# Kernel optimization log

Hardware: AMD Instinct MI355X
Metric: run time of the kernel (lower is better)

The kernel has to match this reference:

```python
import jax, jax.numpy as jnp
import numpy as np


def setup_inputs() -> dict:
    key = jax.random.key(0)
    ks = jax.random.split(key, 10)
    B, L, D_MODEL = 2, 2048, 1024
    D_INNER, N, W, R = 2048, 16, 4, 64
    s = 0.02
    return {
        "hidden_states": jax.random.normal(ks[0], (B, L, D_MODEL), jnp.float32),
        "in_proj_w": jax.random.normal(ks[1], (2 * D_INNER, D_MODEL), jnp.float32) * s,
        "conv_w": jax.random.normal(ks[2], (D_INNER, W), jnp.float32) * 0.2,
        "conv_b": jax.random.normal(ks[3], (D_INNER,), jnp.float32) * 0.02,
        "x_proj_w": jax.random.normal(ks[4], (R + 2 * N, D_INNER), jnp.float32) * s,
        "dt_proj_w": jax.random.normal(ks[5], (D_INNER, R), jnp.float32) * (R ** -0.5),
        "dt_proj_b": jnp.log(jnp.expm1(jnp.exp(jax.random.uniform(ks[6], (D_INNER,), jnp.float32, np.log(1e-3), np.log(1e-1)))) + 1e-20),
        "A_log": jnp.log(jnp.broadcast_to(jnp.arange(1, N + 1, dtype=jnp.float32), (D_INNER, N))),
        "D_param": jnp.ones((D_INNER,), jnp.float32),
        "out_proj_w": jax.random.normal(ks[7], (D_MODEL, D_INNER), jnp.float32) * s,
    }


def _mamba_fwd(hidden_states, in_proj_w, conv_w, conv_b, x_proj_w,
               dt_proj_w, dt_proj_b, A_log, D_param, out_proj_w):
    Bsz, L, _ = hidden_states.shape
    d_inner = conv_w.shape[0]
    n = A_log.shape[1]
    r = dt_proj_w.shape[1]

    # input projection -> x, z  (each [B, L, d_inner])
    xz = jnp.einsum('bld,ed->ble', hidden_states, in_proj_w)
    x, z = xz[..., :d_inner], xz[..., d_inner:]

    # depthwise causal conv over L with SiLU
    x_bdl = jnp.transpose(x, (0, 2, 1))  # [B, d, L]
    kern = conv_w[:, None, :]            # [d, 1, W]
    xc = jax.lax.conv_general_dilated(
        x_bdl, kern, window_strides=(1,), padding=[(conv_w.shape[1] - 1, 0)],
        dimension_numbers=('NCH', 'OIH', 'NCH'), feature_group_count=d_inner)
    xc = xc + conv_b[None, :, None]
    xc = xc * jax.nn.sigmoid(xc)         # silu, [B, d, L]
    u = jnp.transpose(xc, (0, 2, 1))     # [B, L, d]

    # SSM parameter projections
    x_dbl = jnp.einsum('bld,ed->ble', u, x_proj_w)   # [B, L, r+2n]
    dt_lo = x_dbl[..., :r]
    B_ssm = x_dbl[..., r:r + n]                       # [B, L, n]
    C_ssm = x_dbl[..., r + n:]                        # [B, L, n]
    delta = jax.nn.softplus(jnp.einsum('blr,dr->bld', dt_lo, dt_proj_w) + dt_proj_b)

    A = -jnp.exp(A_log)  # [d, n]

    # selective scan over time (sequential recurrence)
    def step(h, inp):
        d_t, u_t, b_t, c_t = inp  # [B,d], [B,d], [B,n], [B,n]
        dA = jnp.exp(d_t[..., None] * A)                       # [B,d,n]
        h = dA * h + (d_t * u_t)[..., None] * b_t[:, None, :]  # [B,d,n]
        y_t = jnp.einsum('bdn,bn->bd', h, c_t)
        return h, y_t

    h0 = jnp.zeros((Bsz, d_inner, n), dtype=u.dtype)
    xs = (jnp.transpose(delta, (1, 0, 2)), jnp.transpose(u, (1, 0, 2)),
          jnp.transpose(B_ssm, (1, 0, 2)), jnp.transpose(C_ssm, (1, 0, 2)))
    _, ys = jax.lax.scan(step, h0, xs)           # ys: [L, B, d]
    y = jnp.transpose(ys, (1, 0, 2)) + u * D_param
    y = y * (z * jax.nn.sigmoid(z))              # gate: y * silu(z)
    return jnp.einsum('bld,ed->ble', y, out_proj_w)


def reference(hidden_states, in_proj_w, conv_w, conv_b, x_proj_w,
              dt_proj_w, dt_proj_b, A_log, D_param, out_proj_w):
    return _mamba_fwd(hidden_states, in_proj_w, conv_w, conv_b, x_proj_w,
                      dt_proj_w, dt_proj_b, A_log, D_param, out_proj_w)
```

## Files before the change

kernel.cpp:

```cpp
#include <hip/hip_runtime.h>
#include <cstdint>
#include <cstddef>

#define Bsz  2
#define Lseq 2048
#define DM   1024
#define DI   2048
#define NS   16
#define RR   64
#define BL   (Bsz * Lseq)
#define TC   64
#define NC   (Lseq / TC)

typedef unsigned short u16;
typedef __attribute__((ext_vector_type(4))) unsigned short u16x4;
typedef __attribute__((ext_vector_type(8))) short short8;
typedef __attribute__((ext_vector_type(4))) float f32x4;

__device__ __forceinline__ u16 f32_to_bf16(float f) {
  union { float f; unsigned int u; } v; v.f = f;
  unsigned int lsb = (v.u >> 16) & 1u;
  v.u += 0x7fffu + lsb;
  return (u16)(v.u >> 16);
}
__device__ __forceinline__ float bf16_to_f32(u16 h) {
  union { unsigned int u; float f; } v; v.u = ((unsigned int)h) << 16;
  return v.f;
}

__global__ void cvt_f32_bf16(const float* __restrict__ src, u16* __restrict__ dst, int n) {
  int i = (blockIdx.x * blockDim.x + threadIdx.x) * 4;
  if (i + 4 <= n) {
    float4 v = *(const float4*)(src + i);
    dst[i + 0] = f32_to_bf16(v.x);
    dst[i + 1] = f32_to_bf16(v.y);
    dst[i + 2] = f32_to_bf16(v.z);
    dst[i + 3] = f32_to_bf16(v.w);
  } else {
    for (; i < n; ++i) dst[i] = f32_to_bf16(src[i]);
  }
}

__global__ void split_bf16_kernel(const float* __restrict__ src,
                                  u16* __restrict__ hi, u16* __restrict__ lo, int n) {
  int i = blockIdx.x * blockDim.x + threadIdx.x;
  if (i >= n) return;
  const float v = src[i];
  const u16 h = f32_to_bf16(v);
  hi[i] = h;
  lo[i] = f32_to_bf16(v - bf16_to_f32(h));
}

__device__ __forceinline__ void gload_lds16(const u16* g, u16* l) {
  __builtin_amdgcn_global_load_lds(
      (const __attribute__((address_space(1))) unsigned int*)g,
      (__attribute__((address_space(3))) unsigned int*)l,
      16, 0, 0);
}

template<bool BF16OUT>
__global__ __launch_bounds__(256) void gemm128_bt(
    const u16* __restrict__ A, const u16* __restrict__ Bt,
    void* __restrict__ outA_, void* __restrict__ outB_,
    int split, int ldA, int ldB, int K, int kstride, size_t zstride)
{
  __shared__ __align__(16) u16 As[128 * 32];
  __shared__ __align__(16) u16 Bs[128 * 32];
  const int tid  = threadIdx.x;
  const int lane = tid & 63;
  const int wid  = tid >> 6;

  const int nwg = gridDim.x * gridDim.y;
  int wg = blockIdx.y * gridDim.x + blockIdx.x;
  wg = (wg & 7) * (nwg >> 3) + (wg >> 3);
  const int m0 = (wg / gridDim.x) * 128;
  const int n0 = (wg % gridDim.x) * 128;
  const int kbase = blockIdx.z * K;

  const int wr = wid >> 1, wc = wid & 1;

  const f32x4 zero = {0.f, 0.f, 0.f, 0.f};
  f32x4 acc[4][4];
#pragma unroll
  for (int i = 0; i < 4; ++i)
#pragma unroll
    for (int j = 0; j < 4; ++j) acc[i][j] = zero;

  const int l16 = lane * 16;

  for (int k0 = 0; k0 < K; k0 += 32) {
    __syncthreads();
#pragma unroll
    for (int c = 0; c < 2; ++c) {
      const int base = c * 4096 + wid * 1024;
      const int ofs  = base + l16;
      const int row  = ofs >> 6;
      const int col  = (ofs >> 1) & 31;
      gload_lds16(A  + (size_t)(m0 + row) * kstride + kbase + k0 + col, (u16*)((char*)As + base));
      gload_lds16(Bt + (size_t)(n0 + row) * kstride + kbase + k0 + col, (u16*)((char*)Bs + base));
    }
    __syncthreads();

    const int kk = (lane >> 4) * 8;
    const int ra = wr * 64 + (lane & 15);
    const int rb = wc * 64 + (lane & 15);
    short8 af[4], bf[4];
#pragma unroll
    for (int i = 0; i < 4; ++i) af[i] = *(const short8*)&As[(ra + i * 16) * 32 + kk];
#pragma unroll
    for (int j = 0; j < 4; ++j) bf[j] = *(const short8*)&Bs[(rb + j * 16) * 32 + kk];
#pragma unroll
    for (int i = 0; i < 4; ++i)
#pragma unroll
      for (int j = 0; j < 4; ++j)
        acc[i][j] = __builtin_amdgcn_mfma_f32_16x16x32_bf16(af[i], bf[j], acc[i][j], 0, 0, 0);
  }

  const bool isA = (n0 < split);
  const int  ld  = isA ? ldA : ldB;
  const int  nb  = isA ? n0 : n0 - split;
  const int cr = (lane >> 4) * 4;
  const int cc = lane & 15;
  if constexpr (BF16OUT) {
    u16* o = (u16*)(isA ? outA_ : outB_);
#pragma unroll
    for (int i = 0; i < 4; ++i)
#pragma unroll
      for (int j = 0; j < 4; ++j)
#pragma unroll
        for (int r = 0; r < 4; ++r) {
          const int m = m0 + wr * 64 + i * 16 + cr + r;
          const int n = nb + wc * 64 + j * 16 + cc;
          o[(size_t)m * ld + n] = f32_to_bf16(acc[i][j][r]);
        }
  } else {
    float* o = (float*)(isA ? outA_ : outB_) + (size_t)blockIdx.z * zstride;
#pragma unroll
    for (int i = 0; i < 4; ++i)
#pragma unroll
      for (int j = 0; j < 4; ++j)
#pragma unroll
        for (int r = 0; r < 4; ++r) {
          const int m = m0 + wr * 64 + i * 16 + cr + r;
          const int n = nb + wc * 64 + j * 16 + cc;
          o[(size_t)m * ld + n] = acc[i][j][r];
        }
  }
}

__global__ void add2_kernel(const float* __restrict__ part, float* __restrict__ out) {
  const int i = (blockIdx.x * blockDim.x + threadIdx.x) * 4;
  const float4 a = *(const float4*)(part + i);
  const float4 b = *(const float4*)(part + (size_t)BL * DM + i);
  float4 s;
  s.x = a.x + b.x; s.y = a.y + b.y; s.z = a.z + b.z; s.w = a.w + b.w;
  *(float4*)(out + i) = s;
}

__global__ __launch_bounds__(256) void gemm_xproj(
    const u16* __restrict__ A, const u16* __restrict__ Bt,
    float* __restrict__ xdbl, u16* __restrict__ dhi, u16* __restrict__ dlo)
{
  const int wg   = blockIdx.x * 4 + (threadIdx.x >> 6);
  const int lane = threadIdx.x & 63;
  const int mt = wg / 6, nt = wg % 6;

  const u16* arow = A  + (size_t)(mt * 16 + (lane & 15)) * DI + ((lane >> 4) * 8);
  const u16* brow = Bt + (size_t)(nt * 16 + (lane & 15)) * DI + ((lane >> 4) * 8);
  f32x4 acc = {0.f, 0.f, 0.f, 0.f};
  for (int k0 = 0; k0 < DI; k0 += 32) {
    short8 a = *(const short8*)(arow + k0);
    short8 b = *(const short8*)(brow + k0);
    acc = __builtin_amdgcn_mfma_f32_16x16x32_bf16(a, b, acc, 0, 0, 0);
  }
  const int cr = (lane >> 4) * 4, cc = lane & 15;
  const int n  = nt * 16 + cc;
#pragma unroll
  for (int r = 0; r < 4; ++r) {
    const int m = mt * 16 + cr + r;
    const float v = acc[r];
    if (n < RR) {
      const u16 h = f32_to_bf16(v);
      dhi[(size_t)m * RR + n] = h;
      dlo[(size_t)m * RR + n] = f32_to_bf16(v - bf16_to_f32(h));
    } else {
      xdbl[(size_t)m * 96 + n] = v;
    }
  }
}

__global__ __launch_bounds__(256) void dt_gemm_mfma(
    const u16* __restrict__ ahi, const u16* __restrict__ alo,
    const u16* __restrict__ bhi, const u16* __restrict__ blo,
    const float* __restrict__ dtb, float* __restrict__ delta)
{
  const int wg   = blockIdx.x * 4 + (threadIdx.x >> 6);
  const int lane = threadIdx.x & 63;
  const int mt = wg >> 7, nt = wg & 127;

  const size_t aofs = (size_t)(mt * 16 + (lane & 15)) * 64 + ((lane >> 4) * 8);
  const size_t bofs = (size_t)(nt * 16 + (lane & 15)) * 64 + ((lane >> 4) * 8);

  f32x4 acc = {0.f, 0.f, 0.f, 0.f};
#pragma unroll
  for (int k0 = 0; k0 < 64; k0 += 32) {
    const short8 Ah = *(const short8*)(ahi + aofs + k0);
    const short8 Al = *(const short8*)(alo + aofs + k0);
    const short8 Bh = *(const short8*)(bhi + bofs + k0);
    const short8 Bl = *(const short8*)(blo + bofs + k0);
    acc = __builtin_amdgcn_mfma_f32_16x16x32_bf16(Ah, Bh, acc, 0, 0, 0);
    acc = __builtin_amdgcn_mfma_f32_16x16x32_bf16(Ah, Bl, acc, 0, 0, 0);
    acc = __builtin_amdgcn_mfma_f32_16x16x32_bf16(Al, Bh, acc, 0, 0, 0);
  }

  const int cr = (lane >> 4) * 4, cc = lane & 15;
  const int n  = nt * 16 + cc;
  const float b = dtb[n];
#pragma unroll
  for (int r = 0; r < 4; ++r) {
    const float s = acc[r] + b;
    const float sp = fmaxf(s, 0.f) + __logf(1.f + __expf(-fabsf(s)));
    delta[(size_t)(mt * 16 + cr + r) * DI + n] = sp;
  }
}

__global__ void conv_silu_kernel(const u16* __restrict__ x,
                                 const float* __restrict__ cw, const float* __restrict__ cb,
                                 u16* __restrict__ ub)
{
  const int idx  = blockIdx.x * blockDim.x + threadIdx.x;
  const int base = idx * 4;
  const int d  = base & (DI - 1);
  const int bl = base >> 11;
  const int l  = bl & (Lseq - 1);
  const u16* xp = x + (size_t)bl * DI + d;
  const u16x4 zv = {0, 0, 0, 0};
  const u16x4 x3 = *(const u16x4*)xp;
  const u16x4 x2 = (l >= 1) ? *(const u16x4*)(xp - DI)     : zv;
  const u16x4 x1 = (l >= 2) ? *(const u16x4*)(xp - 2 * DI) : zv;
  const u16x4 x0 = (l >= 3) ? *(const u16x4*)(xp - 3 * DI) : zv;
  const float4 bias = *(const float4*)&cb[d];
  u16x4 out;
#pragma unroll
  for (int j = 0; j < 4; ++j) {
    const float4 w = *(const float4*)&cw[(d + j) * 4];
    float acc = ((const float*)&bias)[j];
    acc += bf16_to_f32(x0[j]) * w.x + bf16_to_f32(x1[j]) * w.y +
           bf16_to_f32(x2[j]) * w.z + bf16_to_f32(x3[j]) * w.w;
    const float s = acc / (1.f + __expf(-acc));
    out[j] = f32_to_bf16(s);
  }
  *(u16x4*)(ub + (size_t)bl * DI + d) = out;
}


__global__ __launch_bounds__(256) void scan_chunk_ps(
    const float* __restrict__ delta, const u16* __restrict__ u,
    const float* __restrict__ xdbl, const float* __restrict__ alog,
    float* __restrict__ Pout, float* __restrict__ Sout)
{
  __shared__ float Bl[TC][NS];
  const int b   = blockIdx.z;
  const int c   = blockIdx.y;
  const int d   = blockIdx.x * 256 + threadIdx.x;
  const int tid = threadIdx.x;
  const size_t rowBase = (size_t)b * Lseq + (size_t)c * TC;

  {
    const int row = tid >> 2, c4 = (tid & 3) * 4;
    *(float4*)&Bl[row][c4] = *(const float4*)&xdbl[(rowBase + row) * 96 + RR + c4];
  }
  __syncthreads();

  float A[NS];
#pragma unroll
  for (int n4 = 0; n4 < 4; ++n4) {
    const float4 a4 = *(const float4*)&alog[(size_t)d * NS + n4 * 4];
    A[n4 * 4 + 0] = -__expf(a4.x);
    A[n4 * 4 + 1] = -__expf(a4.y);
    A[n4 * 4 + 2] = -__expf(a4.z);
    A[n4 * 4 + 3] = -__expf(a4.w);
  }

  float h[NS], P[NS];
#pragma unroll
  for (int n = 0; n < NS; ++n) { h[n] = 0.f; P[n] = 1.f; }

#pragma unroll 4
  for (int t = 0; t < TC; ++t) {
    const float dt  = delta[(rowBase + t) * DI + d];
    const float ut  = bf16_to_f32(u[(rowBase + t) * DI + d]);
    const float dtu = dt * ut;
#pragma unroll
    for (int n = 0; n < NS; ++n) {
      const float dA = __expf(dt * A[n]);
      P[n] *= dA;
      h[n] = dA * h[n] + dtu * Bl[t][n];
    }
  }

  const size_t base = (size_t)(b * NC + c) * NS * DI + d;
#pragma unroll
  for (int n = 0; n < NS; ++n) {
    Pout[base + (size_t)n * DI] = P[n];
    Sout[base + (size_t)n * DI] = h[n];
  }
}

__global__ __launch_bounds__(256) void scan_combine(
    const float* __restrict__ P, const float* __restrict__ S,
    float* __restrict__ Hin)
{
  const int gid = blockIdx.x * 256 + threadIdx.x;
  const int b   = gid >> 15;
  const int nd  = gid & 32767;
  float h = 0.f;
  for (int c = 0; c < NC; ++c) {
    const size_t o = (size_t)(b * NC + c) * (NS * DI) + nd;
    const float Pc = P[o];
    const float Sc = S[o];
    Hin[o] = h;
    h = Pc * h + Sc;
  }
}

__global__ __launch_bounds__(256) void scan_chunk_y(
    const float* __restrict__ delta, const u16* __restrict__ u,
    const float* __restrict__ xdbl, const float* __restrict__ alog,
    const float* __restrict__ dpar, const u16* __restrict__ z,
    const float* __restrict__ Hin, u16* __restrict__ yb)
{
  __shared__ float Bl[TC][NS];
  __shared__ float Cl[TC][NS];
  const int b   = blockIdx.z;
  const int c   = blockIdx.y;
  const int d   = blockIdx.x * 256 + threadIdx.x;
  const int tid = threadIdx.x;
  const size_t rowBase = (size_t)b * Lseq + (size_t)c * TC;

  {
    const int row = tid >> 2, c4 = (tid & 3) * 4;
    *(float4*)&Bl[row][c4] = *(const float4*)&xdbl[(rowBase + row) * 96 + RR + c4];
    *(float4*)&Cl[row][c4] = *(const float4*)&xdbl[(rowBase + row) * 96 + RR + NS + c4];
  }
  __syncthreads();

  float A[NS];
#pragma unroll
  for (int n4 = 0; n4 < 4; ++n4) {
    const float4 a4 = *(const float4*)&alog[(size_t)d * NS + n4 * 4];
    A[n4 * 4 + 0] = -__expf(a4.x);
    A[n4 * 4 + 1] = -__expf(a4.y);
    A[n4 * 4 + 2] = -__expf(a4.z);
    A[n4 * 4 + 3] = -__expf(a4.w);
  }
  const float Dv = dpar[d];

  float h[NS];
  const size_t sbase = (size_t)(b * NC + c) * NS * DI + d;
#pragma unroll
  for (int n = 0; n < NS; ++n) h[n] = Hin[sbase + (size_t)n * DI];

#pragma unroll 4
  for (int t = 0; t < TC; ++t) {
    const float dt  = delta[(rowBase + t) * DI + d];
    const float ut  = bf16_to_f32(u[(rowBase + t) * DI + d]);
    const float zv  = bf16_to_f32(z[(rowBase + t) * DI + d]);
    const float dtu = dt * ut;
    float y = 0.f;
#pragma unroll
    for (int n = 0; n < NS; ++n) {
      const float dA = __expf(dt * A[n]);
      h[n] = dA * h[n] + dtu * Bl[t][n];
      y += h[n] * Cl[t][n];
    }
    const float yv = y + ut * Dv;
    const float g  = zv / (1.f + __expf(-zv));
    yb[(rowBase + t) * DI + d] = f32_to_bf16(yv * g);
  }
}

extern "C" void kernel_launch(void* const* d_in, const int* in_sizes, int n_in,
                              void* d_out, int out_size, void* d_ws, size_t ws_size,
                              hipStream_t stream)
{
  const float* hs   = (const float*)d_in[0];
  const float* win  = (const float*)d_in[1];
  const float* cw   = (const float*)d_in[2];
  const float* cb   = (const float*)d_in[3];
  const float* wxp  = (const float*)d_in[4];
  const float* wdt  = (const float*)d_in[5];
  const float* bdt  = (const float*)d_in[6];
  const float* alog = (const float*)d_in[7];
  const float* dpar = (const float*)d_in[8];
  const float* wout = (const float*)d_in[9];
  float* out = (float*)d_out;

  char* ws = (char*)d_ws;
  size_t off = 0;
  auto alloc = [&](size_t bytes) -> void* {
    void* p = ws + off;
    off += (bytes + 255) & ~(size_t)255;
    return p;
  };
  u16*   hs_b   = (u16*)  alloc((size_t)BL * DM * 2);
  u16*   win_b  = (u16*)  alloc((size_t)2 * DI * DM * 2);
  u16*   wxp_b  = (u16*)  alloc((size_t)96 * DI * 2);
  u16*   wout_b = (u16*)  alloc((size_t)DM * DI * 2);
  u16*   xbuf   = (u16*)  alloc((size_t)BL * DI * 2);
  u16*   zbuf   = (u16*)  alloc((size_t)BL * DI * 2);
  u16*   ub16   = (u16*)  alloc((size_t)BL * DI * 2);
  float* deltab = (float*)alloc((size_t)BL * DI * 4);
  float* xdbl   = (float*)alloc((size_t)BL * 96 * 4);
  float* Pbuf   = (float*)alloc((size_t)Bsz * NC * DI * NS * 4);
  float* Sbuf   = (float*)alloc((size_t)Bsz * NC * DI * NS * 4);
  u16*   dt_hi  = (u16*)  alloc((size_t)BL * 64 * 2);
  u16*   dt_lo  = (u16*)  alloc((size_t)BL * 64 * 2);
  u16*   w_hi   = (u16*)  alloc((size_t)DI * 64 * 2);
  u16*   w_lo   = (u16*)  alloc((size_t)DI * 64 * 2);
  u16*   y_b    = ub16;
  float* Hin    = Pbuf;
  float* part   = deltab;

  const int thr = 256;
  cvt_f32_bf16<<<(BL * DM / 4 + thr - 1) / thr, thr, 0, stream>>>(hs, hs_b, BL * DM);
  cvt_f32_bf16<<<(2 * DI * DM / 4 + thr - 1) / thr, thr, 0, stream>>>(win, win_b, 2 * DI * DM);
  cvt_f32_bf16<<<(96 * DI / 4 + thr - 1) / thr, thr, 0, stream>>>(wxp, wxp_b, 96 * DI);
  cvt_f32_bf16<<<(DM * DI / 4 + thr - 1) / thr, thr, 0, stream>>>(wout, wout_b, DM * DI);
  split_bf16_kernel<<<(DI * 64) / thr, thr, 0, stream>>>(wdt, w_hi, w_lo, DI * 64);

  {
    dim3 g(4096 / 128, BL / 128);
    gemm128_bt<true><<<g, 256, 0, stream>>>(hs_b, win_b, xbuf, zbuf,
                                            DI, DI, DI, DM, DM, 0);
  }

  conv_silu_kernel<<<(BL * DI / 4) / 256, 256, 0, stream>>>(xbuf, cw, cb, ub16);

  gemm_xproj<<<(256 * 6) / 4, 256, 0, stream>>>(ub16, wxp_b, xdbl, dt_hi, dt_lo);

  dt_gemm_mfma<<<(256 * 128) / 4, 256, 0, stream>>>(dt_hi, dt_lo, w_hi, w_lo, bdt, deltab);

  {
    dim3 gA(DI / 256, NC, Bsz);
    scan_chunk_ps<<<gA, 256, 0, stream>>>(deltab, ub16, xdbl, alog, Pbuf, Sbuf);
    scan_combine<<<(Bsz * DI * NS) / 256, 256, 0, stream>>>(Pbuf, Sbuf, Hin);
    scan_chunk_y<<<gA, 256, 0, stream>>>(deltab, ub16, xdbl, alog, dpar, zbuf, Hin, y_b);
  }

  {
    dim3 g(DM / 128, BL / 128, 2);
    gemm128_bt<false><<<g, 256, 0, stream>>>(y_b, wout_b, part, part,
                                             1 << 30, DM, DM, DI / 2, DI,
                                             (size_t)BL * DM);
    add2_kernel<<<(BL * DM / 4) / 256, 256, 0, stream>>>(part, out);
  }
}
```

Before: 291.8 us.

## Fuse conversion kernels, drop GEMM tile swizzle, keep x/z in fp32

Merges the four bf16 conversion launches and the hi/lo split into one kernel to cut launch overhead. Removes the workgroup swizzle and the bf16-output template from the tiled GEMM, so the in-projection now writes x and z as fp32 and conv and scan read fp32. This doubles the x/z write and read traffic and gives up the L2-friendly tile ordering. In exchange it simplifies the code and gains some precision.

```diff
diff --git a/kernel.cpp b/kernel.cpp
--- a/kernel.cpp
+++ b/kernel.cpp
@@ -28,28 +28,42 @@
   return v.f;
 }
 
-__global__ void cvt_f32_bf16(const float* __restrict__ src, u16* __restrict__ dst, int n) {
+#define N0 (BL * DM)
+#define N1 (2 * DI * DM)
+#define N2 (96 * DI)
+#define N3 (DM * DI)
+#define N4 (DI * 64)
+__global__ __launch_bounds__(256) void cvt_fused(
+    const float* __restrict__ hs, u16* __restrict__ hs_b,
+    const float* __restrict__ win, u16* __restrict__ win_b,
+    const float* __restrict__ wxp, u16* __restrict__ wxp_b,
+    const float* __restrict__ wout, u16* __restrict__ wout_b,
+    const float* __restrict__ wdt, u16* __restrict__ w_hi, u16* __restrict__ w_lo)
+{
   int i = (blockIdx.x * blockDim.x + threadIdx.x) * 4;
-  if (i + 4 <= n) {
-    float4 v = *(const float4*)(src + i);
-    dst[i + 0] = f32_to_bf16(v.x);
-    dst[i + 1] = f32_to_bf16(v.y);
-    dst[i + 2] = f32_to_bf16(v.z);
-    dst[i + 3] = f32_to_bf16(v.w);
-  } else {
-    for (; i < n; ++i) dst[i] = f32_to_bf16(src[i]);
-  }
-}
-
-__global__ void split_bf16_kernel(const float* __restrict__ src,
-                                  u16* __restrict__ hi, u16* __restrict__ lo, int n) {
-  int i = blockIdx.x * blockDim.x + threadIdx.x;
-  if (i >= n) return;
-  const float v = src[i];
-  const u16 h = f32_to_bf16(v);
-  hi[i] = h;
-  lo[i] = f32_to_bf16(v - bf16_to_f32(h));
-}
+  const float* src; u16* dst;
+  if (i < N0)                     { src = hs;   dst = hs_b; }
+  else if ((i -= N0) < N1)        { src = win;  dst = win_b; }
+  else if ((i -= N1) < N2)        { src = wxp;  dst = wxp_b; }
+  else if ((i -= N2) < N3)        { src = wout; dst = wout_b; }
+  else if ((i -= N3) < N4) {
+    const float4 v = *(const float4*)(wdt + i);
+#pragma unroll
+    for (int j = 0; j < 4; ++j) {
+      const float f = ((const float*)&v)[j];
+      const u16 h = f32_to_bf16(f);
+      w_hi[i + j] = h;
+      w_lo[i + j] = f32_to_bf16(f - bf16_to_f32(h));
+    }
+    return;
+  } else return;
+  const float4 v = *(const float4*)(src + i);
+  dst[i + 0] = f32_to_bf16(v.x);
+  dst[i + 1] = f32_to_bf16(v.y);
+  dst[i + 2] = f32_to_bf16(v.z);
+  dst[i + 3] = f32_to_bf16(v.w);
+}
+#define CVT_TOTAL (N0 + N1 + N2 + N3 + N4)
 
 __device__ __forceinline__ void gload_lds16(const u16* g, u16* l) {
   __builtin_amdgcn_global_load_lds(
@@ -58,10 +72,9 @@
       16, 0, 0);
 }
 
-template<bool BF16OUT>
 __global__ __launch_bounds__(256) void gemm128_bt(
     const u16* __restrict__ A, const u16* __restrict__ Bt,
-    void* __restrict__ outA_, void* __restrict__ outB_,
+    float* __restrict__ outA, float* __restrict__ outB,
     int split, int ldA, int ldB, int K, int kstride, size_t zstride)
 {
   __shared__ __align__(16) u16 As[128 * 32];
@@ -69,14 +82,9 @@
   const int tid  = threadIdx.x;
   const int lane = tid & 63;
   const int wid  = tid >> 6;
-
-  const int nwg = gridDim.x * gridDim.y;
-  int wg = blockIdx.y * gridDim.x + blockIdx.x;
-  wg = (wg & 7) * (nwg >> 3) + (wg >> 3);
-  const int m0 = (wg / gridDim.x) * 128;
-  const int n0 = (wg % gridDim.x) * 128;
+  const int m0 = blockIdx.y * 128;
+  const int n0 = blockIdx.x * 128;
   const int kbase = blockIdx.z * K;
-
   const int wr = wid >> 1, wc = wid & 1;
 
   const f32x4 zero = {0.f, 0.f, 0.f, 0.f};
@@ -116,36 +124,20 @@
         acc[i][j] = __builtin_amdgcn_mfma_f32_16x16x32_bf16(af[i], bf[j], acc[i][j], 0, 0, 0);
   }
 
-  const bool isA = (n0 < split);
-  const int  ld  = isA ? ldA : ldB;
-  const int  nb  = isA ? n0 : n0 - split;
   const int cr = (lane >> 4) * 4;
   const int cc = lane & 15;
-  if constexpr (BF16OUT) {
-    u16* o = (u16*)(isA ? outA_ : outB_);
-#pragma unroll
-    for (int i = 0; i < 4; ++i)
-#pragma unroll
-      for (int j = 0; j < 4; ++j)
-#pragma unroll
-        for (int r = 0; r < 4; ++r) {
-          const int m = m0 + wr * 64 + i * 16 + cr + r;
-          const int n = nb + wc * 64 + j * 16 + cc;
-          o[(size_t)m * ld + n] = f32_to_bf16(acc[i][j][r]);
-        }
-  } else {
-    float* o = (float*)(isA ? outA_ : outB_) + (size_t)blockIdx.z * zstride;
-#pragma unroll
-    for (int i = 0; i < 4; ++i)
-#pragma unroll
-      for (int j = 0; j < 4; ++j)
-#pragma unroll
-        for (int r = 0; r < 4; ++r) {
-          const int m = m0 + wr * 64 + i * 16 + cr + r;
-          const int n = nb + wc * 64 + j * 16 + cc;
-          o[(size_t)m * ld + n] = acc[i][j][r];
-        }
-  }
+#pragma unroll
+  for (int i = 0; i < 4; ++i)
+#pragma unroll
+    for (int j = 0; j < 4; ++j)
+#pragma unroll
+      for (int r = 0; r < 4; ++r) {
+        const int m = m0 + wr * 64 + i * 16 + cr + r;
+        const int n = n0 + wc * 64 + j * 16 + cc;
+        const float v = acc[i][j][r];
+        if (n < split) outA[(size_t)m * ldA + n + blockIdx.z * zstride] = v;
+        else           outB[(size_t)m * ldB + (n - split)] = v;
+      }
 }
 
 __global__ void add2_kernel(const float* __restrict__ part, float* __restrict__ out) {
@@ -224,29 +216,30 @@
   }
 }
 
-__global__ void conv_silu_kernel(const u16* __restrict__ x,
-                                 const float* __restrict__ cw, const float* __restrict__ cb,
-                                 u16* __restrict__ ub)
+__global__ __launch_bounds__(256) void conv_silu_kernel(
+    const float* __restrict__ x,
+    const float* __restrict__ cw, const float* __restrict__ cb,
+    u16* __restrict__ ub)
 {
   const int idx  = blockIdx.x * blockDim.x + threadIdx.x;
   const int base = idx * 4;
   const int d  = base & (DI - 1);
   const int bl = base >> 11;
   const int l  = bl & (Lseq - 1);
-  const u16* xp = x + (size_t)bl * DI + d;
-  const u16x4 zv = {0, 0, 0, 0};
-  const u16x4 x3 = *(const u16x4*)xp;
-  const u16x4 x2 = (l >= 1) ? *(const u16x4*)(xp - DI)     : zv;
-  const u16x4 x1 = (l >= 2) ? *(const u16x4*)(xp - 2 * DI) : zv;
-  const u16x4 x0 = (l >= 3) ? *(const u16x4*)(xp - 3 * DI) : zv;
+  const float* xp = x + (size_t)bl * DI + d;
+  const float4 zf = {0.f, 0.f, 0.f, 0.f};
+  const float4 x3 = *(const float4*)xp;
+  const float4 x2 = (l >= 1) ? *(const float4*)(xp - DI)     : zf;
+  const float4 x1 = (l >= 2) ? *(const float4*)(xp - 2 * DI) : zf;
+  const float4 x0 = (l >= 3) ? *(const float4*)(xp - 3 * DI) : zf;
   const float4 bias = *(const float4*)&cb[d];
   u16x4 out;
 #pragma unroll
   for (int j = 0; j < 4; ++j) {
     const float4 w = *(const float4*)&cw[(d + j) * 4];
     float acc = ((const float*)&bias)[j];
-    acc += bf16_to_f32(x0[j]) * w.x + bf16_to_f32(x1[j]) * w.y +
-           bf16_to_f32(x2[j]) * w.z + bf16_to_f32(x3[j]) * w.w;
+    acc += ((const float*)&x0)[j] * w.x + ((const float*)&x1)[j] * w.y +
+           ((const float*)&x2)[j] * w.z + ((const float*)&x3)[j] * w.w;
     const float s = acc / (1.f + __expf(-acc));
     out[j] = f32_to_bf16(s);
   }
@@ -327,7 +320,7 @@
 __global__ __launch_bounds__(256) void scan_chunk_y(
     const float* __restrict__ delta, const u16* __restrict__ u,
     const float* __restrict__ xdbl, const float* __restrict__ alog,
-    const float* __restrict__ dpar, const u16* __restrict__ z,
+    const float* __restrict__ dpar, const float* __restrict__ z,
     const float* __restrict__ Hin, u16* __restrict__ yb)
 {
   __shared__ float Bl[TC][NS];
@@ -365,7 +358,7 @@
   for (int t = 0; t < TC; ++t) {
     const float dt  = delta[(rowBase + t) * DI + d];
     const float ut  = bf16_to_f32(u[(rowBase + t) * DI + d]);
-    const float zv  = bf16_to_f32(z[(rowBase + t) * DI + d]);
+    const float zv  = z[(rowBase + t) * DI + d];
     const float dtu = dt * ut;
     float y = 0.f;
 #pragma unroll
@@ -407,8 +400,8 @@
   u16*   win_b  = (u16*)  alloc((size_t)2 * DI * DM * 2);
   u16*   wxp_b  = (u16*)  alloc((size_t)96 * DI * 2);
   u16*   wout_b = (u16*)  alloc((size_t)DM * DI * 2);
-  u16*   xbuf   = (u16*)  alloc((size_t)BL * DI * 2);
-  u16*   zbuf   = (u16*)  alloc((size_t)BL * DI * 2);
+  float* xbuf   = (float*)alloc((size_t)BL * DI * 4);
+  float* zbuf   = (float*)alloc((size_t)BL * DI * 4);
   u16*   ub16   = (u16*)  alloc((size_t)BL * DI * 2);
   float* deltab = (float*)alloc((size_t)BL * DI * 4);
   float* xdbl   = (float*)alloc((size_t)BL * 96 * 4);
@@ -422,17 +415,13 @@
   float* Hin    = Pbuf;
   float* part   = deltab;
 
-  const int thr = 256;
-  cvt_f32_bf16<<<(BL * DM / 4 + thr - 1) / thr, thr, 0, stream>>>(hs, hs_b, BL * DM);
-  cvt_f32_bf16<<<(2 * DI * DM / 4 + thr - 1) / thr, thr, 0, stream>>>(win, win_b, 2 * DI * DM);
-  cvt_f32_bf16<<<(96 * DI / 4 + thr - 1) / thr, thr, 0, stream>>>(wxp, wxp_b, 96 * DI);
-  cvt_f32_bf16<<<(DM * DI / 4 + thr - 1) / thr, thr, 0, stream>>>(wout, wout_b, DM * DI);
-  split_bf16_kernel<<<(DI * 64) / thr, thr, 0, stream>>>(wdt, w_hi, w_lo, DI * 64);
+  cvt_fused<<<(CVT_TOTAL / 4 + 255) / 256, 256, 0, stream>>>(
+      hs, hs_b, win, win_b, wxp, wxp_b, wout, wout_b, wdt, w_hi, w_lo);
 
   {
     dim3 g(4096 / 128, BL / 128);
-    gemm128_bt<true><<<g, 256, 0, stream>>>(hs_b, win_b, xbuf, zbuf,
-                                            DI, DI, DI, DM, DM, 0);
+    gemm128_bt<<<g, 256, 0, stream>>>(hs_b, win_b, xbuf, zbuf,
+                                      DI, DI, DI, DM, DM, 0);
   }
 
   conv_silu_kernel<<<(BL * DI / 4) / 256, 256, 0, stream>>>(xbuf, cw, cb, ub16);
@@ -450,9 +439,9 @@
 
   {
     dim3 g(DM / 128, BL / 128, 2);
-    gemm128_bt<false><<<g, 256, 0, stream>>>(y_b, wout_b, part, part,
-                                             1 << 30, DM, DM, DI / 2, DI,
-                                             (size_t)BL * DM);
+    gemm128_bt<<<g, 256, 0, stream>>>(y_b, wout_b, part, part,
+                                      1 << 30, DM, DM, DI / 2, DI,
+                                      (size_t)BL * DM);
     add2_kernel<<<(BL * DM / 4) / 256, 256, 0, stream>>>(part, out);
   }
 }
```

Result: no change. 296.3 us (+1.5%).
